# Kernel tuning notes

Measured on AMD Instinct MI355X. Metric: run time of the kernel, lower is better.

The kernel has to match this reference:

```python
import jax, jax.numpy as jnp
import numpy as np

D_MODEL = 2816
N_HEADS = 16
DH = 512
N_KV = 2
MAX_CTX = 8192
POS = 4095  # current decode position (0-indexed)
EPS = 1e-6
Q_DIM = N_HEADS * DH
KV_DIM = N_KV * DH
NEG_INF = -1e9


def setup_inputs() -> dict:
    key = jax.random.key(0)
    ks = jax.random.split(key, 8)
    x = jax.random.normal(ks[0], (1, 1, D_MODEL), jnp.float32)
    # Realistic RoPE angles at position POS (full head_dim rotation, half/half layout)
    inv_freq = 1.0 / (10000.0 ** (np.arange(0, DH, 2, dtype=np.float32) / DH))  # (DH/2,)
    ang = POS * inv_freq
    cos = jnp.asarray(np.concatenate([np.cos(ang), np.cos(ang)])[None, None, :], jnp.float32)  # (1,1,DH)
    sin = jnp.asarray(np.concatenate([np.sin(ang), np.sin(ang)])[None, None, :], jnp.float32)
    k_cache = jax.random.normal(ks[1], (1, N_KV, MAX_CTX, DH), jnp.float32) * 0.02
    v_cache = jax.random.normal(ks[2], (1, N_KV, MAX_CTX, DH), jnp.float32) * 0.02
    # causal decode mask: attend to [0, POS], -inf beyond
    pos_ids = jnp.arange(MAX_CTX)
    attn_mask = jnp.where(pos_ids <= POS, 0.0, NEG_INF).astype(jnp.float32).reshape(1, 1, 1, MAX_CTX)
    # one-hot write mask at current position
    kv_write_mask = jnp.zeros((1, 1, MAX_CTX, 1), jnp.float32).at[0, 0, POS, 0].set(1.0)
    Wq = jax.random.normal(ks[3], (Q_DIM, D_MODEL), jnp.float32) * 0.02
    Wk = jax.random.normal(ks[4], (KV_DIM, D_MODEL), jnp.float32) * 0.02
    Wo = jax.random.normal(ks[5], (D_MODEL, Q_DIM), jnp.float32) * 0.02
    q_gamma = jax.random.normal(ks[6], (DH,), jnp.float32) * 0.02  # stored as (gamma-1)
    k_gamma = jax.random.normal(ks[7], (DH,), jnp.float32) * 0.02
    return {"x": x, "cos": cos, "sin": sin, "k_cache": k_cache, "v_cache": v_cache,
            "attn_mask": attn_mask, "kv_write_mask": kv_write_mask,
            "Wq": Wq, "Wk": Wk, "Wo": Wo, "q_gamma": q_gamma, "k_gamma": k_gamma}


def _rmsnorm(x, w=None):
    v = jnp.mean(x * x, axis=-1, keepdims=True)
    x = x * jax.lax.rsqrt(v + EPS)
    return x if w is None else x * (1.0 + w)


def _rope(x, cos, sin):
    # x: (1,T,H,D); cos/sin: (1,T,D)
    c = cos[:, :, None, :]
    s = sin[:, :, None, :]
    d = x.shape[-1]
    x1, x2 = x[..., : d // 2], x[..., d // 2 :]
    rot = jnp.concatenate([-x2, x1], axis=-1)
    return x * c + rot * s


def reference(x, cos, sin, k_cache, v_cache, attn_mask, kv_write_mask, Wq, Wk, Wo, q_gamma, k_gamma):
    q_raw = (x @ Wq.T).reshape(1, 1, N_HEADS, DH)
    k_raw = (x @ Wk.T).reshape(1, 1, N_KV, DH)
    q = _rope(_rmsnorm(q_raw, q_gamma), cos, sin)
    k = _rope(_rmsnorm(k_raw, k_gamma), cos, sin)
    v = _rmsnorm(k_raw)  # unscaled norm, not rotated
    q = jnp.swapaxes(q, 1, 2)  # (1,H,1,D)
    k = jnp.swapaxes(k, 1, 2)  # (1,n_kv,1,D)
    v = jnp.swapaxes(v, 1, 2)
    k_new = k_cache + k * kv_write_mask  # broadcast write at current slot
    v_new = v_cache + v * kv_write_mask
    rep = N_HEADS // N_KV
    K = jnp.repeat(k_new, rep, axis=1)  # (1,H,S,D)
    V = jnp.repeat(v_new, rep, axis=1)
    scores = jnp.einsum("bhtd,bhsd->bhts", q, K) + attn_mask  # no 1/sqrt(d) scale, as in source
    w = jax.nn.softmax(scores.astype(jnp.float32), axis=-1).astype(q.dtype)
    ctx = jnp.einsum("bhts,bhsd->bhtd", w, V)  # (1,H,1,D)
    ctx = jnp.swapaxes(ctx, 1, 2).reshape(1, 1, Q_DIM)
    out = ctx @ Wo.T
    return (out, k_new, v_new)
```

## Files before the change

kernel.cpp:

```cpp
#include <hip/hip_runtime.h>
#include <math.h>

#define D_MODEL 2816
#define N_HEADS 16
#define DH      512
#define N_KV    2
#define MAX_CTX 8192
#define POS     4095
#define EPS     1e-6f
#define Q_DIM   8192
#define KV_DIM  1024
#define GROUP   8
#define NPOS    4096

#define NB_MV   1152
#define NB_CP   512


typedef float nfloat4 __attribute__((ext_vector_type(4)));

__device__ __forceinline__ float4 f4_mul(float4 a, float s) {
  return make_float4(a.x*s, a.y*s, a.z*s, a.w*s);
}
__device__ __forceinline__ float4 f4_mul4(float4 a, float4 b) {
  return make_float4(a.x*b.x, a.y*b.y, a.z*b.z, a.w*b.w);
}
__device__ __forceinline__ float4 f4_fma(float4 a, float4 b, float4 c) {
  return make_float4(fmaf(a.x,b.x,c.x), fmaf(a.y,b.y,c.y), fmaf(a.z,b.z,c.z), fmaf(a.w,b.w,c.w));
}
__device__ __forceinline__ float4 f4_fmas(float s, float4 b, float4 c) {
  return make_float4(fmaf(s,b.x,c.x), fmaf(s,b.y,c.y), fmaf(s,b.z,c.z), fmaf(s,b.w,c.w));
}
__device__ __forceinline__ float4 f4_fnma(float4 a, float4 b, float4 c) {
  return make_float4(fmaf(-a.x,b.x,c.x), fmaf(-a.y,b.y,c.y), fmaf(-a.z,b.z,c.z), fmaf(-a.w,b.w,c.w));
}
__device__ __forceinline__ float4 f4_add(float4 a, float4 b) {
  return make_float4(a.x+b.x, a.y+b.y, a.z+b.z, a.w+b.w);
}
__device__ __forceinline__ float f4_dot(float4 a, float4 b) {
  return a.x*b.x + a.y*b.y + a.z*b.z + a.w*b.w;
}
__device__ __forceinline__ float f4_ssq(float4 a) {
  return a.x*a.x + a.y*a.y + a.z*a.z + a.w*a.w;
}
__device__ __forceinline__ float4 ntl(const float4* p) {
  nfloat4 v = __builtin_nontemporal_load(reinterpret_cast<const nfloat4*>(p));
  return make_float4(v.x, v.y, v.z, v.w);
}
__device__ __forceinline__ void nts(float4* p, float4 v) {
  nfloat4 nv; nv.x = v.x; nv.y = v.y; nv.z = v.z; nv.w = v.w;
  __builtin_nontemporal_store(nv, reinterpret_cast<nfloat4*>(p));
}

__global__ __launch_bounds__(256) void k_a(const float* __restrict__ x,
    const float* __restrict__ Wq, const float* __restrict__ Wk,
    const float* __restrict__ kc, const float* __restrict__ vc,
    float* __restrict__ knew, float* __restrict__ vnew,
    float* __restrict__ qraw, float* __restrict__ kraw,
    float* __restrict__ ctx, float* __restrict__ lvec) {
  int t = threadIdx.x;
  int blk = blockIdx.x;
  int w = t >> 6, lane = t & 63;
  if (blk == 0) {
    float4* c4 = (float4*)ctx;
#pragma unroll
    for (int j = 0; j < 8; ++j) c4[j * 256 + t] = make_float4(0.f, 0.f, 0.f, 0.f);
    if (t < 16) lvec[t] = 0.f;
  }
  if (blk < NB_MV) {
    const float4* x4 = (const float4*)x;
    int W = blk * 4 + w;
#pragma unroll
    for (int i = 0; i < 2; ++i) {
      int row = W + i * 4608;
      const float4* W4 = (row < Q_DIM)
          ? (const float4*)(Wq + (size_t)row * D_MODEL)
          : (const float4*)(Wk + (size_t)(row - Q_DIM) * D_MODEL);
      float a0 = 0.f, a1 = 0.f;
#pragma unroll
      for (int it = 0; it < D_MODEL / 256; ++it) {
        float d = f4_dot(ntl(&W4[it * 64 + lane]), x4[it * 64 + lane]);
        if (it & 1) a1 += d; else a0 += d;
      }
      float acc = a0 + a1;
#pragma unroll
      for (int m = 32; m; m >>= 1) acc += __shfl_xor(acc, m, 64);
      if (lane == 0) {
        if (row < Q_DIM) qraw[row] = acc;
        else             kraw[row - Q_DIM] = acc;
      }
    }
  } else {
    int idx = blk - NB_MV;
#pragma unroll
    for (int r = 0; r < 4; ++r) {
      int u = idx * 16 + w * 4 + r;
      int g = u >> 12;
      int s = 4096 + (u & 4095);
      size_t row = ((size_t)g * MAX_CTX + s) * DH;
      const float4* kc4 = (const float4*)(kc + row);
      const float4* vc4 = (const float4*)(vc + row);
      float4* ko4 = (float4*)(knew + row);
      float4* vo4 = (float4*)(vnew + row);
      nts(&ko4[lane],      ntl(&kc4[lane]));
      nts(&ko4[64 + lane], ntl(&kc4[64 + lane]));
      nts(&vo4[lane],      ntl(&vc4[lane]));
      nts(&vo4[64 + lane], ntl(&vc4[64 + lane]));
    }
  }
}

__global__ __launch_bounds__(512) void k_att(
    const float* __restrict__ kc, const float* __restrict__ vc,
    const float* __restrict__ qraw, const float* __restrict__ kraw,
    const float* __restrict__ cosv, const float* __restrict__ sinv,
    const float* __restrict__ qg,   const float* __restrict__ kg,
    float* __restrict__ knew, float* __restrict__ vnew,
    float* __restrict__ ctx, float* __restrict__ lvec) {
  __shared__ float4 lq[GROUP * 128];
  __shared__ float  pvbuf[8 * 512];
  __shared__ float  lbuf[64];
  __shared__ float4 kfin[128];
  __shared__ float4 vfin[128];
  int b = blockIdx.x;
  int g = b >> 7;
  int rb = b & 127;
  int t = threadIdx.x;
  int w = t >> 6, lane = t & 63;

  {
    const float4* c4 = (const float4*)cosv;
    const float4* s4 = (const float4*)sinv;
    float4 c1 = c4[lane],      s1 = s4[lane];
    float4 c2 = c4[64 + lane], s2 = s4[64 + lane];
    const float4* qr4 = (const float4*)(qraw + (size_t)(g * GROUP + w) * DH);
    float4 a  = qr4[lane];
    float4 b2 = qr4[64 + lane];
    float ss = f4_ssq(a) + f4_ssq(b2);
#pragma unroll
    for (int m = 32; m; m >>= 1) ss += __shfl_xor(ss, m, 64);
    float scale = rsqrtf(ss * (1.f / (float)DH) + EPS);
    const float4* qg4 = (const float4*)qg;
    float4 ga = qg4[lane], gb = qg4[64 + lane];
    float4 na = f4_mul4(f4_mul(a,  scale), make_float4(1.f+ga.x,1.f+ga.y,1.f+ga.z,1.f+ga.w));
    float4 nb = f4_mul4(f4_mul(b2, scale), make_float4(1.f+gb.x,1.f+gb.y,1.f+gb.z,1.f+gb.w));
    lq[w * 128 + lane]      = f4_fnma(nb, s1, f4_mul4(na, c1));
    lq[w * 128 + 64 + lane] = f4_fma (na, s2, f4_mul4(nb, c2));
    if (rb == (POS >> 5) && w == 0) {
      const float4* kr4 = (const float4*)(kraw + (size_t)g * DH);
      float4 ka_ = kr4[lane];
      float4 kb_ = kr4[64 + lane];
      float ss2 = f4_ssq(ka_) + f4_ssq(kb_);
#pragma unroll
      for (int m = 32; m; m >>= 1) ss2 += __shfl_xor(ss2, m, 64);
      float sc2 = rsqrtf(ss2 * (1.f / (float)DH) + EPS);
      float4 va_ = f4_mul(ka_, sc2);
      float4 vb_ = f4_mul(kb_, sc2);
      const float4* kg4 = (const float4*)kg;
      float4 ga2 = kg4[lane], gb2 = kg4[64 + lane];
      float4 na2 = f4_mul4(va_, make_float4(1.f+ga2.x,1.f+ga2.y,1.f+ga2.z,1.f+ga2.w));
      float4 nb2 = f4_mul4(vb_, make_float4(1.f+gb2.x,1.f+gb2.y,1.f+gb2.z,1.f+gb2.w));
      kfin[lane]      = f4_fnma(nb2, s1, f4_mul4(na2, c1));
      kfin[64 + lane] = f4_fma (na2, s2, f4_mul4(nb2, c2));
      vfin[lane]      = va_;
      vfin[64 + lane] = vb_;
    }
    __syncthreads();
  }

  float4 acc[GROUP][2];
#pragma unroll
  for (int h = 0; h < GROUP; ++h) { acc[h][0] = make_float4(0,0,0,0); acc[h][1] = make_float4(0,0,0,0); }
  float lacc[GROUP] = {0.f,0.f,0.f,0.f,0.f,0.f,0.f,0.f};

  for (int r = 0; r < 4; ++r) {
    int s = (rb << 5) + (w << 2) + r;
    size_t row = ((size_t)g * MAX_CTX + s) * DH;
    const float4* kc4 = (const float4*)(kc + row);
    const float4* vc4 = (const float4*)(vc + row);
    float4 ka = ntl(&kc4[lane]), kb = ntl(&kc4[64 + lane]);
    float4 va = ntl(&vc4[lane]), vb = ntl(&vc4[64 + lane]);
    if (s == POS) {
      ka = f4_add(ka, kfin[lane]); kb = f4_add(kb, kfin[64 + lane]);
      va = f4_add(va, vfin[lane]); vb = f4_add(vb, vfin[64 + lane]);
    }
    float4* ko4 = (float4*)(knew + row);
    float4* vo4 = (float4*)(vnew + row);
    nts(&ko4[lane], ka); nts(&ko4[64 + lane], kb);
    nts(&vo4[lane], va); nts(&vo4[64 + lane], vb);
    float sc[GROUP];
#pragma unroll
    for (int h = 0; h < GROUP; ++h)
      sc[h] = f4_dot(lq[h * 128 + lane], ka) + f4_dot(lq[h * 128 + 64 + lane], kb);
#pragma unroll
    for (int h = 0; h < GROUP; ++h) {
#pragma unroll
      for (int m = 32; m; m >>= 1) sc[h] += __shfl_xor(sc[h], m, 64);
    }
#pragma unroll
    for (int h = 0; h < GROUP; ++h) {
      float e = __expf(fminf(sc[h], 80.f));
      lacc[h] += e;
      acc[h][0] = f4_fmas(e, va, acc[h][0]);
      acc[h][1] = f4_fmas(e, vb, acc[h][1]);
    }
  }

  {
    float4* pv4 = (float4*)pvbuf;
#pragma unroll
    for (int h = 0; h < GROUP; ++h) {
      __syncthreads();
      pv4[w * 128 + lane]      = acc[h][0];
      pv4[w * 128 + 64 + lane] = acc[h][1];
      __syncthreads();
      float sum = 0.f;
#pragma unroll
      for (int w2 = 0; w2 < 8; ++w2) sum += pvbuf[w2 * 512 + t];
      atomicAdd(&ctx[(size_t)(g * GROUP + h) * DH + t], sum);
    }
    float myl = 0.f;
#pragma unroll
    for (int h = 0; h < GROUP; ++h) myl = (lane == h) ? lacc[h] : myl;
    if (lane < 8) lbuf[w * 8 + lane] = myl;
    __syncthreads();
    if (t < 8) {
      float sl = 0.f;
#pragma unroll
      for (int w2 = 0; w2 < 8; ++w2) sl += lbuf[w2 * 8 + t];
      atomicAdd(&lvec[g * GROUP + t], sl);
    }
  }
}

__global__ __launch_bounds__(256) void k_oproj(const float* __restrict__ ctx,
    const float* __restrict__ lvec, const float* __restrict__ Wo,
    float* __restrict__ out) {
  __shared__ float linv[16];
  int t = threadIdx.x;
  if (t < 16) linv[t] = 1.f / lvec[t];
  __syncthreads();
  int wid  = (blockIdx.x * blockDim.x + t) >> 6;
  int lane = t & 63;
  const float4* c4 = (const float4*)ctx;
  int row = wid;
  const float4* W4 = (const float4*)(Wo + (size_t)row * Q_DIM);
  float a0 = 0.f, a1 = 0.f;
#pragma unroll
  for (int it = 0; it < Q_DIM / 256; ++it) {
    float d = f4_dot(ntl(&W4[it * 64 + lane]), c4[it * 64 + lane]) * linv[it >> 1];
    if (it & 1) a1 += d; else a0 += d;
  }
  float acc = a0 + a1;
#pragma unroll
  for (int m = 32; m; m >>= 1) acc += __shfl_xor(acc, m, 64);
  if (lane == 0) out[row] = acc;
}

extern "C" void kernel_launch(void* const* d_in, const int* in_sizes, int n_in,
                              void* d_out, int out_size, void* d_ws, size_t ws_size,
                              hipStream_t stream) {
  (void)in_sizes; (void)n_in; (void)out_size; (void)ws_size;
  const float* x    = (const float*)d_in[0];
  const float* cosv = (const float*)d_in[1];
  const float* sinv = (const float*)d_in[2];
  const float* kc   = (const float*)d_in[3];
  const float* vc   = (const float*)d_in[4];
  const float* Wq   = (const float*)d_in[7];
  const float* Wk   = (const float*)d_in[8];
  const float* Wo   = (const float*)d_in[9];
  const float* qg   = (const float*)d_in[10];
  const float* kg   = (const float*)d_in[11];

  float* out  = (float*)d_out;
  float* knew = out + D_MODEL;
  float* vnew = knew + (size_t)N_KV * MAX_CTX * DH;

  float* w      = (float*)d_ws;
  float* qraw   = w;
  float* kraw   = w + 8192;
  float* ctx    = w + 9216;
  float* lvec   = w + 17408;

  k_a    <<<NB_MV + NB_CP, 256, 0, stream>>>(x, Wq, Wk, kc, vc, knew, vnew,
                                             qraw, kraw, ctx, lvec);
  k_att  <<<256, 512, 0, stream>>>(kc, vc, qraw, kraw, cosv, sinv, qg, kg,
                                   knew, vnew, ctx, lvec);
  k_oproj<<<704, 256, 0, stream>>>(ctx, lvec, Wo, out);
}
```

Before: 70.43 us.

## Interleave QK matvec rows, halve copy work per block, split Wo rows across warps

The Q/K projection now computes its two rows per warp in one interleaved loop that shares the x loads, so more independent loads are in flight. The cache-tail copy uses twice as many blocks, each copying half as many rows. The output projection splits each Wo row across two warps and combines the halves through shared memory, doubling the block count. The aim is more memory-level parallelism and better occupancy across all three memory-bound phases, at the cost of more register pressure and an extra sync in k_oproj.

```diff
diff --git a/kernel.cpp b/kernel.cpp
--- a/kernel.cpp
+++ b/kernel.cpp
@@ -14,7 +14,7 @@
 #define NPOS    4096
 
 #define NB_MV   1152
-#define NB_CP   512
+#define NB_CP   1024
 
 
 typedef float nfloat4 __attribute__((ext_vector_type(4)));
@@ -70,31 +70,38 @@
   if (blk < NB_MV) {
     const float4* x4 = (const float4*)x;
     int W = blk * 4 + w;
-#pragma unroll
-    for (int i = 0; i < 2; ++i) {
-      int row = W + i * 4608;
-      const float4* W4 = (row < Q_DIM)
-          ? (const float4*)(Wq + (size_t)row * D_MODEL)
-          : (const float4*)(Wk + (size_t)(row - Q_DIM) * D_MODEL);
-      float a0 = 0.f, a1 = 0.f;
-#pragma unroll
-      for (int it = 0; it < D_MODEL / 256; ++it) {
-        float d = f4_dot(ntl(&W4[it * 64 + lane]), x4[it * 64 + lane]);
-        if (it & 1) a1 += d; else a0 += d;
-      }
-      float acc = a0 + a1;
-#pragma unroll
-      for (int m = 32; m; m >>= 1) acc += __shfl_xor(acc, m, 64);
-      if (lane == 0) {
-        if (row < Q_DIM) qraw[row] = acc;
-        else             kraw[row - Q_DIM] = acc;
-      }
+    int rowA = W;
+    int rowB = W + 4608;
+    const float4* A4 = (const float4*)(Wq + (size_t)rowA * D_MODEL);
+    const float4* B4 = (rowB < Q_DIM)
+        ? (const float4*)(Wq + (size_t)rowB * D_MODEL)
+        : (const float4*)(Wk + (size_t)(rowB - Q_DIM) * D_MODEL);
+    float a0 = 0.f, a1 = 0.f, b0 = 0.f, b1 = 0.f;
+#pragma unroll
+    for (int it = 0; it < D_MODEL / 256; ++it) {
+      float4 xv = x4[it * 64 + lane];
+      float4 wa = ntl(&A4[it * 64 + lane]);
+      float4 wb = ntl(&B4[it * 64 + lane]);
+      float da = f4_dot(wa, xv);
+      float db = f4_dot(wb, xv);
+      if (it & 1) { a1 += da; b1 += db; } else { a0 += da; b0 += db; }
+    }
+    float accA = a0 + a1, accB = b0 + b1;
+#pragma unroll
+    for (int m = 32; m; m >>= 1) {
+      accA += __shfl_xor(accA, m, 64);
+      accB += __shfl_xor(accB, m, 64);
+    }
+    if (lane == 0) {
+      qraw[rowA] = accA;
+      if (rowB < Q_DIM) qraw[rowB] = accB;
+      else              kraw[rowB - Q_DIM] = accB;
     }
   } else {
     int idx = blk - NB_MV;
 #pragma unroll
-    for (int r = 0; r < 4; ++r) {
-      int u = idx * 16 + w * 4 + r;
+    for (int r = 0; r < 2; ++r) {
+      int u = idx * 8 + w * 2 + r;
       int g = u >> 12;
       int s = 4096 + (u & 4095);
       size_t row = ((size_t)g * MAX_CTX + s) * DH;
@@ -237,24 +244,28 @@
     const float* __restrict__ lvec, const float* __restrict__ Wo,
     float* __restrict__ out) {
   __shared__ float linv[16];
+  __shared__ float rsum[4];
   int t = threadIdx.x;
   if (t < 16) linv[t] = 1.f / lvec[t];
   __syncthreads();
-  int wid  = (blockIdx.x * blockDim.x + t) >> 6;
-  int lane = t & 63;
+  int w = t >> 6, lane = t & 63;
+  int row = blockIdx.x * 2 + (w >> 1);
   const float4* c4 = (const float4*)ctx;
-  int row = wid;
   const float4* W4 = (const float4*)(Wo + (size_t)row * Q_DIM);
+  int it0 = (w & 1) * 16;
   float a0 = 0.f, a1 = 0.f;
 #pragma unroll
-  for (int it = 0; it < Q_DIM / 256; ++it) {
+  for (int i = 0; i < 16; ++i) {
+    int it = it0 + i;
     float d = f4_dot(ntl(&W4[it * 64 + lane]), c4[it * 64 + lane]) * linv[it >> 1];
-    if (it & 1) a1 += d; else a0 += d;
+    if (i & 1) a1 += d; else a0 += d;
   }
   float acc = a0 + a1;
 #pragma unroll
   for (int m = 32; m; m >>= 1) acc += __shfl_xor(acc, m, 64);
-  if (lane == 0) out[row] = acc;
+  if (lane == 0) rsum[w] = acc;
+  __syncthreads();
+  if ((w & 1) == 0 && lane == 0) out[row] = rsum[w] + rsum[w + 1];
 }
 
 extern "C" void kernel_launch(void* const* d_in, const int* in_sizes, int n_in,
@@ -286,5 +297,5 @@
                                              qraw, kraw, ctx, lvec);
   k_att  <<<256, 512, 0, stream>>>(kc, vc, qraw, kraw, cosv, sinv, qg, kg,
                                    knew, vnew, ctx, lvec);
-  k_oproj<<<704, 256, 0, stream>>>(ctx, lvec, Wo, out);
-}
+  k_oproj<<<1408, 256, 0, stream>>>(ctx, lvec, Wo, out);
+}
```

New measurement: 68.56 us (median of 2 runs). -2.7%, faster.
